# Kernel tuning notes

Measured on AMD Instinct MI355X. Metric: run time of the kernel, lower is better.

The kernel has to match this reference:

```python
import jax, jax.numpy as jnp
import numpy as np

N, ID, OD, M, S, L = 65536, 16, 8, 1024, 8, 64


def setup_inputs() -> dict:
    key = jax.random.key(0)
    k1, k2, k3, k4, k5, k6 = jax.random.split(key, 6)
    return {
        "x": jax.random.normal(k1, (N, ID), dtype=jnp.float32),
        "inducing_locations": jax.random.uniform(k2, (M, ID), dtype=jnp.float32),
        "inducing_weights": jax.random.normal(k3, (S, OD, M), dtype=jnp.float32),
        "prior_frequency": jax.random.normal(k4, (OD, ID, L), dtype=jnp.float32),
        "prior_phase": jax.random.uniform(k5, (OD, L), dtype=jnp.float32, maxval=2 * np.pi),
        "prior_weights": jax.random.normal(k6, (S, OD, L), dtype=jnp.float32),
    }


def _rbf_matrix(x, z):
    # ExponentiatedQuadratic with amplitude=1, length_scale=1:
    # k(x,z) = exp(-0.5 * ||x - z||^2)
    x2 = jnp.sum(x * x, axis=-1)[:, None]          # [N,1]
    z2 = jnp.sum(z * z, axis=-1)[None, :]          # [1,M]
    sq = jnp.maximum(x2 + z2 - 2.0 * (x @ z.T), 0.0)
    return jnp.exp(-0.5 * sq)                      # [N,M]


def reference(x, inducing_locations, inducing_weights, prior_frequency, prior_phase, prior_weights):
    # ---- prior (random Fourier features) ----
    # spectral_weights for unit RBF: outer_weights = ones((OD,L)), inner_weights = ones((ID,))
    # rescaled_x = x / 1 = x
    # basis_fn_inner_prod: [OD, N, L]
    inner = jnp.einsum('ni,oil->onl', x, prior_frequency)
    basis_fn = jnp.cos(inner + prior_phase[:, None, :])              # [OD,N,L]
    basis_weight = jnp.sqrt(2.0 / prior_frequency.shape[-1]) * prior_weights  # [S,OD,L]
    f_prior = jnp.einsum('onl,sol->son', basis_fn, basis_weight)     # [S,OD,N]

    # ---- data term (kernel matrix + matvec) ----
    K = _rbf_matrix(x, inducing_locations)                           # [N,M]
    f_data = jnp.einsum('nm,som->son', K, inducing_weights)          # [S,OD,N]

    return f_prior + f_data
```

## Files before the change

### kernel.cpp

```cpp
#include <hip/hip_runtime.h>
#include <hip/hip_bf16.h>

#define N_PTS 65536
#define LOG2E 1.4426950408889634f

typedef __attribute__((ext_vector_type(8))) short short8;
typedef __attribute__((ext_vector_type(4))) float float4v;

#if __has_builtin(__builtin_amdgcn_exp2f)
#define EXP2F(x) __builtin_amdgcn_exp2f(x)
#else
#define EXP2F(x) exp2f(x)
#endif

__device__ __forceinline__ short f2b(float f) {
    __hip_bfloat16 h = __float2bfloat16(f);
    return *(short*)&h;
}
__device__ __forceinline__ float b2f(short s) {
    __hip_bfloat16 h = *(__hip_bfloat16*)&s;
    return __bfloat162float(h);
}

__global__ __launch_bounds__(256) void prep_kernel(
    const float* __restrict__ z, const float* __restrict__ W,
    const float* __restrict__ F, const float* __restrict__ pw,
    short* __restrict__ zb, short* __restrict__ FbB,
    short* __restrict__ BWd, short* __restrict__ Wtb,
    float* __restrict__ z2h)
{
    int t = blockIdx.x * 256 + threadIdx.x;
    if (t < 16384) {
        zb[t] = f2b(LOG2E * z[t]);
    } else if (t < 17408) {
        int m = t - 16384;
        const float4v* zp = (const float4v*)(z + (size_t)m * 16);
        float s = 0.f;
        #pragma unroll
        for (int k = 0; k < 4; k++) {
            float4v v = zp[k];
            float a0 = b2f(f2b(v.x)), a1 = b2f(f2b(v.y));
            float a2 = b2f(f2b(v.z)), a3 = b2f(f2b(v.w));
            s += a0 * a0 + a1 * a1 + a2 * a2 + a3 * a3;
        }
        z2h[m] = 0.5f * LOG2E * s;
    } else if (t < 25600) {
        int p = t - 17408;
        int o = p >> 10, l = (p >> 4) & 63, i = p & 15;
        FbB[p] = f2b(F[o * 1024 + i * 64 + l]);
    } else if (t < 58368) {
        int p = t - 25600;
        int so = p >> 9, ol = p & 511, o = ol >> 6;
        float v = ((so & 7) == o) ? 0.17677669529663687f * pw[so * 64 + (ol & 63)] : 0.f;
        BWd[p] = f2b(v);
    } else if (t < 123904) {
        int p = t - 58368;
        Wtb[p] = f2b(W[p]);
    }
}

__global__ __launch_bounds__(256, 4) void fused_kernel(
    const float* __restrict__ x, const float* __restrict__ ph,
    const short* __restrict__ zb, const short* __restrict__ FbB,
    const short* __restrict__ BWd, const short* __restrict__ Wtb,
    const float* __restrict__ z2h, float* __restrict__ out)
{
    __shared__ __align__(16) short tile[2][64 * 136];
    __shared__ float phc[512];
    __shared__ float x2c[64];

    const int tid = threadIdx.x;
    const int lane = tid & 63, w = tid >> 6;
    const int q = lane >> 4, c = lane & 15;
    const int n0 = blockIdx.x * 64;

    for (int i = tid; i < 512; i += 256) phc[i] = ph[i];
    if (tid < 64) {
        float s = 0.f;
        const float4v* xr = (const float4v*)(x + (size_t)(n0 + tid) * 16);
        #pragma unroll
        for (int k = 0; k < 4; k++) {
            float4v v = xr[k];
            float a0 = b2f(f2b(v.x)), a1 = b2f(f2b(v.y));
            float a2 = b2f(f2b(v.z)), a3 = b2f(f2b(v.w));
            s += a0 * a0 + a1 * a1 + a2 * a2 + a3 * a3;
        }
        x2c[tid] = 0.5f * LOG2E * s;
    }

    short8 ax = (short8)0;
    if (q < 2) {
        const float4v* xp = (const float4v*)(x + (size_t)(n0 + 16 * w + c) * 16 + q * 8);
        float4v v0 = xp[0], v1 = xp[1];
        ax[0] = f2b(v0.x); ax[1] = f2b(v0.y); ax[2] = f2b(v0.z); ax[3] = f2b(v0.w);
        ax[4] = f2b(v1.x); ax[5] = f2b(v1.y); ax[6] = f2b(v1.z); ax[7] = f2b(v1.w);
    }

    float4v acc[4];
    #pragma unroll
    for (int i = 0; i < 4; i++) acc[i] = (float4v)(0.f);

    __syncthreads();

    #pragma unroll
    for (int p = 0; p < 4; p++) {
        short* tl = tile[p & 1];
        #pragma unroll
        for (int lt = 0; lt < 8; lt++) {
            short8 bf = (short8)0;
            if (q < 2) bf = *(const short8*)(FbB + ((p * 128 + lt * 16 + c) * 16 + q * 8));
            float phv = phc[p * 128 + lt * 16 + c];
            float4v c0 = {phv, phv, phv, phv};
            float4v d = __builtin_amdgcn_mfma_f32_16x16x32_bf16(ax, bf, c0, 0, 0, 0);
            #pragma unroll
            for (int r = 0; r < 4; r++)
                tl[(16 * w + q * 4 + r) * 136 + lt * 16 + c] = f2b(__cosf(d[r]));
        }
        short8 aw[4];
        #pragma unroll
        for (int ks = 0; ks < 4; ks++)
            aw[ks] = *(const short8*)(BWd + ((16 * w + c) * 512 + p * 128 + ks * 32 + q * 8));
        __syncthreads();
        #pragma unroll
        for (int ks = 0; ks < 4; ks++) {
            #pragma unroll
            for (int nt = 0; nt < 4; nt++) {
                short8 bb = *(const short8*)(tl + (nt * 16 + c) * 136 + ks * 32 + q * 8);
                acc[nt] = __builtin_amdgcn_mfma_f32_16x16x32_bf16(aw[ks], bb, acc[nt], 0, 0, 0);
            }
        }
    }

    float mx2[4];
    #pragma unroll
    for (int r = 0; r < 4; r++) mx2[r] = -x2c[16 * w + q * 4 + r];

    #pragma unroll
    for (int mc = 0; mc < 8; mc++) {
        short* tl = tile[mc & 1];
        int m0 = mc * 128;
        #pragma unroll
        for (int mt = 0; mt < 8; mt++) {
            short8 bz = (short8)0;
            if (q < 2) bz = *(const short8*)(zb + ((m0 + mt * 16 + c) * 16 + q * 8));
            float z2v = z2h[m0 + mt * 16 + c];
            float4v c0;
            #pragma unroll
            for (int r = 0; r < 4; r++) c0[r] = mx2[r] - z2v;
            float4v d = __builtin_amdgcn_mfma_f32_16x16x32_bf16(ax, bz, c0, 0, 0, 0);
            #pragma unroll
            for (int r = 0; r < 4; r++)
                tl[(16 * w + q * 4 + r) * 136 + mt * 16 + c] = f2b(EXP2F(d[r]));
        }
        short8 aw[4];
        #pragma unroll
        for (int ks = 0; ks < 4; ks++)
            aw[ks] = *(const short8*)(Wtb + ((16 * w + c) * 1024 + m0 + ks * 32 + q * 8));
        __syncthreads();
        #pragma unroll
        for (int ks = 0; ks < 4; ks++) {
            #pragma unroll
            for (int nt = 0; nt < 4; nt++) {
                short8 bb = *(const short8*)(tl + (nt * 16 + c) * 136 + ks * 32 + q * 8);
                acc[nt] = __builtin_amdgcn_mfma_f32_16x16x32_bf16(aw[ks], bb, acc[nt], 0, 0, 0);
            }
        }
    }

    #pragma unroll
    for (int nt = 0; nt < 4; nt++) {
        #pragma unroll
        for (int r = 0; r < 4; r++) {
            out[(size_t)(16 * w + q * 4 + r) * N_PTS + n0 + nt * 16 + c] = acc[nt][r];
        }
    }
}

extern "C" void kernel_launch(void* const* d_in, const int* in_sizes, int n_in,
                              void* d_out, int out_size, void* d_ws, size_t ws_size,
                              hipStream_t stream) {
    const float* x  = (const float*)d_in[0];
    const float* z  = (const float*)d_in[1];
    const float* W  = (const float*)d_in[2];
    const float* F  = (const float*)d_in[3];
    const float* ph = (const float*)d_in[4];
    const float* pw = (const float*)d_in[5];
    float* out = (float*)d_out;

    char* ws = (char*)d_ws;
    short* zb  = (short*)(ws);
    short* FbB = (short*)(ws + 32768);
    short* BWd = (short*)(ws + 49152);
    short* Wtb = (short*)(ws + 114688);
    float* z2h = (float*)(ws + 245760);

    prep_kernel<<<484, 256, 0, stream>>>(z, W, F, pw, zb, FbB, BWd, Wtb, z2h);
    fused_kernel<<<1024, 256, 0, stream>>>(x, ph, zb, FbB, BWd, Wtb, z2h, out);
}
```

Before: 123.3 us.

## Split reduction dimension across warps with private LDS tiles and final cross-warp reduce

Each warp now computes all 64 outputs for the block but over its own quarter of the inducing points and Fourier features. The kernel-matrix and cosine tiles go into a per-warp swizzled LDS region, which removes the per-chunk block-wide barriers. Partial accumulators from the four warps are summed through LDS at the end. The exp(-x²/2) factor is pulled out of the exponent and applied once to the accumulators. This adds more accumulator registers (launch bounds relaxed to 3 blocks per SM) and some reduction overhead, and the unscaled bf16 exponentials could lose some precision.

```diff
diff --git a/kernel.cpp b/kernel.cpp
--- a/kernel.cpp
+++ b/kernel.cpp
@@ -5,6 +5,7 @@
 #define LOG2E 1.4426950408889634f
 
 typedef __attribute__((ext_vector_type(8))) short short8;
+typedef __attribute__((ext_vector_type(4))) short short4v;
 typedef __attribute__((ext_vector_type(4))) float float4v;
 
 #if __has_builtin(__builtin_amdgcn_exp2f)
@@ -59,15 +60,19 @@
     }
 }
 
-__global__ __launch_bounds__(256, 4) void fused_kernel(
+__global__ __launch_bounds__(256, 3) void fused_kernel(
     const float* __restrict__ x, const float* __restrict__ ph,
     const short* __restrict__ zb, const short* __restrict__ FbB,
     const short* __restrict__ BWd, const short* __restrict__ Wtb,
     const float* __restrict__ z2h, float* __restrict__ out)
 {
-    __shared__ __align__(16) short tile[2][64 * 136];
-    __shared__ float phc[512];
-    __shared__ float x2c[64];
+    __shared__ __align__(16) char smem[34816];
+    short* tiles = (short*)smem;
+    float* phc   = (float*)(smem + 16384);
+    float* nz2   = (float*)(smem + 18432);
+    float* x2c   = (float*)(smem + 22528);
+    float* rbufA = (float*)smem;
+    float* rbufB = (float*)(smem + 17408);
 
     const int tid = threadIdx.x;
     const int lane = tid & 63, w = tid >> 6;
@@ -75,6 +80,7 @@
     const int n0 = blockIdx.x * 64;
 
     for (int i = tid; i < 512; i += 256) phc[i] = ph[i];
+    for (int i = tid; i < 1024; i += 256) nz2[i] = -z2h[i];
     if (tid < 64) {
         float s = 0.f;
         const float4v* xr = (const float4v*)(x + (size_t)(n0 + tid) * 16);
@@ -88,91 +94,135 @@
         x2c[tid] = 0.5f * LOG2E * s;
     }
 
-    short8 ax = (short8)0;
-    if (q < 2) {
-        const float4v* xp = (const float4v*)(x + (size_t)(n0 + 16 * w + c) * 16 + q * 8);
-        float4v v0 = xp[0], v1 = xp[1];
-        ax[0] = f2b(v0.x); ax[1] = f2b(v0.y); ax[2] = f2b(v0.z); ax[3] = f2b(v0.w);
-        ax[4] = f2b(v1.x); ax[5] = f2b(v1.y); ax[6] = f2b(v1.z); ax[7] = f2b(v1.w);
-    }
-
-    float4v acc[4];
-    #pragma unroll
-    for (int i = 0; i < 4; i++) acc[i] = (float4v)(0.f);
-
-    __syncthreads();
-
-    #pragma unroll
-    for (int p = 0; p < 4; p++) {
-        short* tl = tile[p & 1];
-        #pragma unroll
-        for (int lt = 0; lt < 8; lt++) {
+    short8 ax[4];
+    #pragma unroll
+    for (int nt = 0; nt < 4; nt++) {
+        ax[nt] = (short8)0;
+        if (q < 2) {
+            const float4v* xp = (const float4v*)(x + (size_t)(n0 + nt * 16 + c) * 16 + q * 8);
+            float4v v0 = xp[0], v1 = xp[1];
+            ax[nt][0] = f2b(v0.x); ax[nt][1] = f2b(v0.y);
+            ax[nt][2] = f2b(v0.z); ax[nt][3] = f2b(v0.w);
+            ax[nt][4] = f2b(v1.x); ax[nt][5] = f2b(v1.y);
+            ax[nt][6] = f2b(v1.z); ax[nt][7] = f2b(v1.w);
+        }
+    }
+
+    float4v acc[4][4];
+    #pragma unroll
+    for (int a = 0; a < 4; a++)
+        #pragma unroll
+        for (int nt = 0; nt < 4; nt++) acc[a][nt] = (float4v)(0.f);
+
+    __syncthreads();
+
+    char* myt = (char*)tiles + w * 4096;
+    const int swz = (c & 3) << 4;
+    const int wb0 = (c * 64 + q * 8) ^ swz;
+    const int wb1 = (c * 64 + 32 + q * 8) ^ swz;
+    const int rb0 = (c * 64 + q * 16) ^ swz;
+
+    const int mbase = w * 256;
+    #pragma unroll 2
+    for (int mb = 0; mb < 8; mb++) {
+        const int m0 = mbase + mb * 32;
+        #pragma unroll
+        for (int mh = 0; mh < 2; mh++) {
+            short8 bz = (short8)0;
+            if (q < 2) bz = *(const short8*)(zb + (size_t)(m0 + mh * 16 + c) * 16 + q * 8);
+            float4v c0 = *(const float4v*)(nz2 + m0 + mh * 16 + 4 * q);
+            const int wb = mh ? wb1 : wb0;
+            #pragma unroll
+            for (int nt = 0; nt < 4; nt++) {
+                float4v d = __builtin_amdgcn_mfma_f32_16x16x32_bf16(bz, ax[nt], c0, 0, 0, 0);
+                short4v pk;
+                pk[0] = f2b(EXP2F(d[0])); pk[1] = f2b(EXP2F(d[1]));
+                pk[2] = f2b(EXP2F(d[2])); pk[3] = f2b(EXP2F(d[3]));
+                *(short4v*)(myt + nt * 1024 + wb) = pk;
+            }
+        }
+        short8 aw[4];
+        #pragma unroll
+        for (int a = 0; a < 4; a++)
+            aw[a] = *(const short8*)(Wtb + (size_t)(a * 16 + c) * 1024 + m0 + q * 8);
+        #pragma unroll
+        for (int nt = 0; nt < 4; nt++) {
+            short8 bb = *(const short8*)(myt + nt * 1024 + rb0);
+            #pragma unroll
+            for (int a = 0; a < 4; a++)
+                acc[a][nt] = __builtin_amdgcn_mfma_f32_16x16x32_bf16(aw[a], bb, acc[a][nt], 0, 0, 0);
+        }
+    }
+
+    #pragma unroll
+    for (int nt = 0; nt < 4; nt++) {
+        float sxv = EXP2F(-x2c[nt * 16 + c]);
+        #pragma unroll
+        for (int a = 0; a < 4; a++) acc[a][nt] *= sxv;
+    }
+
+    const int lbase = w * 128;
+    #pragma unroll 2
+    for (int lb = 0; lb < 4; lb++) {
+        const int l0 = lbase + lb * 32;
+        #pragma unroll
+        for (int mh = 0; mh < 2; mh++) {
             short8 bf = (short8)0;
-            if (q < 2) bf = *(const short8*)(FbB + ((p * 128 + lt * 16 + c) * 16 + q * 8));
-            float phv = phc[p * 128 + lt * 16 + c];
-            float4v c0 = {phv, phv, phv, phv};
-            float4v d = __builtin_amdgcn_mfma_f32_16x16x32_bf16(ax, bf, c0, 0, 0, 0);
-            #pragma unroll
-            for (int r = 0; r < 4; r++)
-                tl[(16 * w + q * 4 + r) * 136 + lt * 16 + c] = f2b(__cosf(d[r]));
+            if (q < 2) bf = *(const short8*)(FbB + (size_t)(l0 + mh * 16 + c) * 16 + q * 8);
+            float4v c0 = *(const float4v*)(phc + l0 + mh * 16 + 4 * q);
+            const int wb = mh ? wb1 : wb0;
+            #pragma unroll
+            for (int nt = 0; nt < 4; nt++) {
+                float4v d = __builtin_amdgcn_mfma_f32_16x16x32_bf16(bf, ax[nt], c0, 0, 0, 0);
+                short4v pk;
+                pk[0] = f2b(__cosf(d[0])); pk[1] = f2b(__cosf(d[1]));
+                pk[2] = f2b(__cosf(d[2])); pk[3] = f2b(__cosf(d[3]));
+                *(short4v*)(myt + nt * 1024 + wb) = pk;
+            }
         }
         short8 aw[4];
         #pragma unroll
-        for (int ks = 0; ks < 4; ks++)
-            aw[ks] = *(const short8*)(BWd + ((16 * w + c) * 512 + p * 128 + ks * 32 + q * 8));
-        __syncthreads();
-        #pragma unroll
-        for (int ks = 0; ks < 4; ks++) {
-            #pragma unroll
-            for (int nt = 0; nt < 4; nt++) {
-                short8 bb = *(const short8*)(tl + (nt * 16 + c) * 136 + ks * 32 + q * 8);
-                acc[nt] = __builtin_amdgcn_mfma_f32_16x16x32_bf16(aw[ks], bb, acc[nt], 0, 0, 0);
-            }
-        }
-    }
-
-    float mx2[4];
-    #pragma unroll
-    for (int r = 0; r < 4; r++) mx2[r] = -x2c[16 * w + q * 4 + r];
-
-    #pragma unroll
-    for (int mc = 0; mc < 8; mc++) {
-        short* tl = tile[mc & 1];
-        int m0 = mc * 128;
-        #pragma unroll
-        for (int mt = 0; mt < 8; mt++) {
-            short8 bz = (short8)0;
-            if (q < 2) bz = *(const short8*)(zb + ((m0 + mt * 16 + c) * 16 + q * 8));
-            float z2v = z2h[m0 + mt * 16 + c];
-            float4v c0;
-            #pragma unroll
-            for (int r = 0; r < 4; r++) c0[r] = mx2[r] - z2v;
-            float4v d = __builtin_amdgcn_mfma_f32_16x16x32_bf16(ax, bz, c0, 0, 0, 0);
-            #pragma unroll
-            for (int r = 0; r < 4; r++)
-                tl[(16 * w + q * 4 + r) * 136 + mt * 16 + c] = f2b(EXP2F(d[r]));
-        }
-        short8 aw[4];
-        #pragma unroll
-        for (int ks = 0; ks < 4; ks++)
-            aw[ks] = *(const short8*)(Wtb + ((16 * w + c) * 1024 + m0 + ks * 32 + q * 8));
-        __syncthreads();
-        #pragma unroll
-        for (int ks = 0; ks < 4; ks++) {
-            #pragma unroll
-            for (int nt = 0; nt < 4; nt++) {
-                short8 bb = *(const short8*)(tl + (nt * 16 + c) * 136 + ks * 32 + q * 8);
-                acc[nt] = __builtin_amdgcn_mfma_f32_16x16x32_bf16(aw[ks], bb, acc[nt], 0, 0, 0);
-            }
-        }
-    }
-
-    #pragma unroll
-    for (int nt = 0; nt < 4; nt++) {
-        #pragma unroll
-        for (int r = 0; r < 4; r++) {
-            out[(size_t)(16 * w + q * 4 + r) * N_PTS + n0 + nt * 16 + c] = acc[nt][r];
-        }
+        for (int a = 0; a < 4; a++)
+            aw[a] = *(const short8*)(BWd + (size_t)(a * 16 + c) * 512 + l0 + q * 8);
+        #pragma unroll
+        for (int nt = 0; nt < 4; nt++) {
+            short8 bb = *(const short8*)(myt + nt * 1024 + rb0);
+            #pragma unroll
+            for (int a = 0; a < 4; a++)
+                acc[a][nt] = __builtin_amdgcn_mfma_f32_16x16x32_bf16(aw[a], bb, acc[a][nt], 0, 0, 0);
+        }
+    }
+
+    __syncthreads();
+    if (w & 1) {
+        float* rb = (w == 1) ? rbufA : rbufB;
+        #pragma unroll
+        for (int a = 0; a < 4; a++)
+            #pragma unroll
+            for (int nt = 0; nt < 4; nt++)
+                #pragma unroll
+                for (int r = 0; r < 4; r++)
+                    rb[(a * 16 + 4 * q + r) * 68 + nt * 16 + c] = acc[a][nt][r];
+    }
+    __syncthreads();
+    if (!(w & 1)) {
+        float* rb = (w == 0) ? rbufA : rbufB;
+        #pragma unroll
+        for (int a = 0; a < 4; a++)
+            #pragma unroll
+            for (int nt = 0; nt < 4; nt++)
+                #pragma unroll
+                for (int r = 0; r < 4; r++) {
+                    int idx = (a * 16 + 4 * q + r) * 68 + nt * 16 + c;
+                    rb[idx] += acc[a][nt][r];
+                }
+    }
+    __syncthreads();
+    #pragma unroll
+    for (int k = 0; k < 16; k++) {
+        int idx = k * 256 + tid;
+        int row = idx >> 6, nn = idx & 63;
+        out[(size_t)row * N_PTS + n0 + nn] = rbufA[row * 68 + nn] + rbufB[row * 68 + nn];
     }
 }
 
```

New measurement: 108.6 us. 1.14x faster.
